# Kernel tuning notes

Hardware: AMD Instinct MI355X
Metric: run time of the kernel (lower is better)

Reference implementation:

```python
import jax, jax.numpy as jnp
import numpy as np

N = 50000   # nodes
E = 600000  # edges (avg degree ~12)
R = 8       # num_relations = 2 * n_speakers**2, n_speakers=2
B = 32      # num_bases = args.batch_size
GD, H1, H2 = 128, 128, 128


def setup_inputs() -> dict:
    key = jax.random.key(0)
    ks = jax.random.split(key, 16)
    w = lambda k, shape: jax.random.normal(k, shape, jnp.float32) * 0.05
    return {
        "node_features": jax.random.normal(ks[0], (N, GD), jnp.float32),
        "edge_index": jax.random.randint(ks[1], (2, E), 0, N),
        "edge_norm": jax.random.uniform(ks[2], (E,), jnp.float32),
        "edge_type": jax.random.randint(ks[3], (E,), 0, R),
        "basis": w(ks[4], (B, GD, H1)),
        "comp": w(ks[5], (R, B)),
        "root": w(ks[6], (GD, H1)),
        "bias1": jnp.zeros((H1,), jnp.float32),
        "w_key": w(ks[7], (H1, H2)),
        "b_key": jnp.zeros((H2,), jnp.float32),
        "w_query": w(ks[8], (H1, H2)),
        "b_query": jnp.zeros((H2,), jnp.float32),
        "w_value": w(ks[9], (H1, H2)),
        "b_value": jnp.zeros((H2,), jnp.float32),
        "w_skip": w(ks[10], (H1, H2)),
        "b_skip": jnp.zeros((H2,), jnp.float32),
    }


def reference(node_features, edge_index, edge_norm, edge_type, basis, comp,
              root, bias1, w_key, b_key, w_query, b_query, w_value, b_value,
              w_skip, b_skip):
    n = node_features.shape[0]
    r = comp.shape[0]
    src, dst = edge_index[0], edge_index[1]

    # ---- RGCNConv (basis decomposition, per-relation mean aggregation) ----
    W = jnp.einsum('rb,bio->rio', comp, basis)            # [R, GD, H1]
    xW = jnp.einsum('ni,rio->rno', node_features, W)      # [R, N, H1]
    msg = xW[edge_type, src]                              # [E, H1]
    seg = edge_type * n + dst                             # combined (relation, dst) segment id
    agg = jax.ops.segment_sum(msg, seg, num_segments=r * n).reshape(r, n, -1)
    cnt = jax.ops.segment_sum(jnp.ones(msg.shape[0], jnp.float32), seg,
                              num_segments=r * n).reshape(r, n, 1)
    h = (agg / jnp.maximum(cnt, 1.0)).sum(0) + node_features @ root + bias1

    # ---- ResGatedGraphConv: sigmoid(k_i + q_j) * v_j, sum-aggregated + skip ----
    k = h @ w_key + b_key
    q = h @ w_query + b_query
    v = h @ w_value + b_value
    m = jax.nn.sigmoid(k[dst] + q[src]) * v[src]          # [E, H2]
    out = jax.ops.segment_sum(m, dst, num_segments=n) + h @ w_skip + b_skip
    return out
```

## Files before the change

### kernel.cpp

```cpp
#include <hip/hip_runtime.h>
#include <stdint.h>

#define GD 128
#define H1 128
#define H2 128
#define NBASES 32
#define NREL 8
#define KZ 1152

typedef __attribute__((ext_vector_type(8))) short bf16x8;
typedef __attribute__((ext_vector_type(4))) float f32x4;

static inline size_t align256(size_t x){ return (x + 255) & ~(size_t)255; }

__device__ __forceinline__ float bf2f(uint32_t u16){
  union { uint32_t u; float f; } c; c.u = (u16 & 0xffffu) << 16; return c.f;
}
__device__ __forceinline__ unsigned short f2bf(float f){
  union { float f; uint32_t u; } c; c.f = f;
  uint32_t u = c.u;
  u += 0x7fffu + ((u >> 16) & 1u);
  return (unsigned short)(u >> 16);
}
__device__ __forceinline__ uint32_t pkbf(float a, float b){
  union { float f; uint32_t u; } ca, cb; ca.f = a; cb.f = b;
  return __builtin_amdgcn_perm(cb.u + 0x8000u, ca.u + 0x8000u, 0x07060302u);
}

__device__ __forceinline__ void async_copy16(void* lds_dst, const void* gsrc){
  __builtin_amdgcn_global_load_lds(
      (const __attribute__((address_space(1))) uint32_t*)gsrc,
      (__attribute__((address_space(3))) uint32_t*)lds_dst, 16, 0, 0);
}

__global__ void k_prep(const float* __restrict__ comp, const float* __restrict__ basis,
                       const float* __restrict__ root, unsigned short* __restrict__ Bz,
                       const float* __restrict__ wk, const float* __restrict__ wq,
                       const float* __restrict__ wv, const float* __restrict__ wsk,
                       const float* __restrict__ bk, const float* __restrict__ bq,
                       const float* __restrict__ bv, const float* __restrict__ bs,
                       unsigned short* __restrict__ B2t, float* __restrict__ Bb,
                       const float4* __restrict__ x, uint2* __restrict__ xout, int cnt4,
                       uint32_t* __restrict__ xpadz, int npadz,
                       const int* __restrict__ edst, const int* __restrict__ etyp,
                       int* __restrict__ cnt, int E, int n){
  int b = blockIdx.x, t = threadIdx.x;
  if (b < 576){
    int idx = b*256 + t;
    int row = idx >> 7, i = idx & 127;
    int r = row >> 7, o = row & 127;
    float v;
    if (r < 8){
      float acc = 0.f;
      #pragma unroll
      for (int bb = 0; bb < NBASES; ++bb)
        acc += comp[r*NBASES + bb] * basis[((size_t)bb*GD + i)*H1 + o];
      v = acc;
    } else {
      v = root[(size_t)i*H1 + o];
    }
    Bz[idx] = f2bf(v);
  } else if (b < 576 + 256){
    int idx = (b - 576)*256 + t;
    int c = idx / H1, k = idx % H1;
    const float* w = (c < 128) ? wk : (c < 256) ? wq : (c < 384) ? wv : wsk;
    B2t[idx] = f2bf(w[(size_t)k*H2 + (c & 127)]);
    if (idx < 512){
      const float* bia = (idx < 128) ? bk : (idx < 256) ? bq : (idx < 384) ? bv : bs;
      Bb[idx] = bia[idx & 127];
    }
  } else {
    int cb = b - (576 + 256);
    int ncastb = (cnt4 + 255) >> 8;
    if (cb < ncastb){
      int i = cb*256 + t;
      if (i < cnt4){
        float4 v = x[i];
        uint2 o; o.x = pkbf(v.x, v.y); o.y = pkbf(v.z, v.w);
        xout[i] = o;
      }
    } else if (cb < ncastb + 12){
      int i = (cb - ncastb)*256 + t;
      if (i < npadz) xpadz[i] = 0u;
    } else {
      int e = (cb - ncastb - 12)*256 + t;
      if (e < E) atomicAdd(&cnt[etyp[e]*n + edst[e]], 1);
    }
  }
}

__global__ void k_scanA(const int* __restrict__ deg, int* __restrict__ off,
                        int* __restrict__ btot, int len){
  __shared__ int wsum[16];
  int t = threadIdx.x, lane = t & 63, w = t >> 6;
  int i0 = blockIdx.x*8192 + t*8;
  int v[8];
  if (i0 + 7 < len){
    int4 va = *(const int4*)(deg + i0);
    int4 vb = *(const int4*)(deg + i0 + 4);
    v[0]=va.x; v[1]=va.y; v[2]=va.z; v[3]=va.w;
    v[4]=vb.x; v[5]=vb.y; v[6]=vb.z; v[7]=vb.w;
  } else {
    #pragma unroll
    for (int u = 0; u < 8; ++u) v[u] = (i0+u < len) ? deg[i0+u] : 0;
  }
  int s[8]; s[0] = v[0];
  #pragma unroll
  for (int u = 1; u < 8; ++u) s[u] = s[u-1] + v[u];
  int x = s[7];
  #pragma unroll
  for (int d = 1; d < 64; d <<= 1){
    int u = __shfl_up(x, d, 64);
    if (lane >= d) x += u;
  }
  if (lane == 63) wsum[w] = x;
  __syncthreads();
  if (t < 16){
    int y = wsum[t];
    #pragma unroll
    for (int d = 1; d < 16; d <<= 1){
      int u = __shfl_up(y, d, 16);
      if (t >= d) y += u;
    }
    wsum[t] = y;
  }
  __syncthreads();
  int woff = (w > 0) ? wsum[w-1] : 0;
  int excl = woff + x - s[7];
  #pragma unroll
  for (int u = 0; u < 8; ++u)
    if (i0+u < len) off[i0+u] = excl + s[u] - v[u];
  if (t == 0) btot[blockIdx.x] = wsum[15];
}

__global__ void k_scanB(const int* __restrict__ btot, int* __restrict__ off,
                        int* __restrict__ cursor, int len, int sentinel){
  int t = threadIdx.x, bid = blockIdx.x;
  int add = 0;
  for (int j = 0; j < bid; ++j) add += btot[j];
  int i0 = bid*8192 + t*8;
  #pragma unroll
  for (int u = 0; u < 8; ++u){
    int i = i0 + u;
    if (i < len){ int val = off[i] + add; off[i] = val; cursor[i] = val; }
  }
  if (bid == 0 && t == 0) off[len] = sentinel;
}

__global__ void k_scatter_rd(const int* __restrict__ src, const int* __restrict__ dst,
                             const int* __restrict__ typ, int* __restrict__ cursor,
                             int* __restrict__ pk, int E, int n){
  int e = blockIdx.x*blockDim.x + threadIdx.x;
  if (e >= E) return;
  int pos = atomicAdd(&cursor[typ[e]*n + dst[e]], 1);
  pk[pos] = src[e];
}

__launch_bounds__(256)
__global__ void k_zgemm(const unsigned short* __restrict__ A, const unsigned short* __restrict__ Bt,
                        unsigned short* __restrict__ Z){
  __shared__ char lds[16384];
  int t = threadIdx.x, lane = t & 63, wave = t >> 6;
  int row0 = blockIdx.x * 128;
  int c0 = blockIdx.y * 128;
  int mrow = lane & 15, quad = lane >> 4;
  int wrow = (wave & 1) * 64, wcol = (wave >> 1) * 64;
  int s = (mrow >> 1) & 3;

  const unsigned short* Asrc = A + (size_t)(row0 + (t >> 2))*H1 + (((t & 3) ^ ((t >> 3) & 3)) << 3);
  const unsigned short* Bsrc = Bt + (size_t)(c0 + (t >> 2))*H1 + (((t & 3) ^ ((t >> 3) & 3)) << 3);
  char* ldsw = lds + wave*1024;

  int aoff = (wrow + mrow)*64 + ((quad ^ s) << 4);
  int boff = 8192 + (wcol + mrow)*64 + ((quad ^ s) << 4);

  f32x4 acc[4][4];
  #pragma unroll
  for (int i = 0; i < 4; ++i)
    #pragma unroll
    for (int j = 0; j < 4; ++j) acc[i][j] = (f32x4){0.f,0.f,0.f,0.f};

  #pragma unroll
  for (int kt = 0; kt < H1; kt += 32){
    __syncthreads();
    async_copy16(ldsw,         Asrc + kt);
    async_copy16(ldsw + 4096,  Asrc + (size_t)64*H1 + kt);
    async_copy16(ldsw + 8192,  Bsrc + kt);
    async_copy16(ldsw + 12288, Bsrc + (size_t)64*H1 + kt);
    __syncthreads();
    bf16x8 af[4], bf[4];
    #pragma unroll
    for (int i = 0; i < 4; ++i) af[i] = *(const bf16x8*)(lds + aoff + i*1024);
    #pragma unroll
    for (int j = 0; j < 4; ++j) bf[j] = *(const bf16x8*)(lds + boff + j*1024);
    #pragma unroll
    for (int i = 0; i < 4; ++i)
      #pragma unroll
      for (int j = 0; j < 4; ++j)
        acc[i][j] = __builtin_amdgcn_mfma_f32_16x16x32_bf16(af[i], bf[j], acc[i][j], 0, 0, 0);
  }
  #pragma unroll
  for (int j = 0; j < 4; ++j){
    int col = c0 + wcol + j*16 + mrow;
    #pragma unroll
    for (int i = 0; i < 4; ++i)
      #pragma unroll
      for (int rg = 0; rg < 4; ++rg){
        int row = row0 + wrow + i*16 + quad*4 + rg;
        Z[(size_t)row*KZ + col] = f2bf(acc[i][j][rg]);
      }
  }
}

__global__ void k_edge1(const int* __restrict__ off_rd, const int* __restrict__ pk_rd,
                        const unsigned short* __restrict__ Zb,
                        const float* __restrict__ bias1,
                        unsigned short* __restrict__ h, int n, int npad){
  int wid = blockIdx.x*(blockDim.x >> 6) + (threadIdx.x >> 6);
  int lane = threadIdx.x & 63;
  if (wid >= npad) return;
  uint32_t* hrow = (uint32_t*)(h + (size_t)wid*H1);
  if (wid >= n){ hrow[lane] = 0u; return; }
  const uint32_t* Z32 = (const uint32_t*)Zb;
  int r8 = lane & 7;
  int o_r = off_rd[(size_t)r8*n + wid];
  int e_r = off_rd[(size_t)r8*n + wid + 1];
  int c_r = e_r - o_r;
  float ic_r = (c_r > 0) ? (1.f/(float)c_r) : 0.f;
  int c0_ = __builtin_amdgcn_readlane(c_r, 0), c1_ = __builtin_amdgcn_readlane(c_r, 1);
  int c2_ = __builtin_amdgcn_readlane(c_r, 2), c3_ = __builtin_amdgcn_readlane(c_r, 3);
  int c4_ = __builtin_amdgcn_readlane(c_r, 4), c5_ = __builtin_amdgcn_readlane(c_r, 5);
  int c6_ = __builtin_amdgcn_readlane(c_r, 6), c7_ = __builtin_amdgcn_readlane(c_r, 7);
  int o0_ = __builtin_amdgcn_readlane(o_r, 0), o1_ = __builtin_amdgcn_readlane(o_r, 1);
  int o2_ = __builtin_amdgcn_readlane(o_r, 2), o3_ = __builtin_amdgcn_readlane(o_r, 3);
  int o4_ = __builtin_amdgcn_readlane(o_r, 4), o5_ = __builtin_amdgcn_readlane(o_r, 5);
  int o6_ = __builtin_amdgcn_readlane(o_r, 6), o7_ = __builtin_amdgcn_readlane(o_r, 7);
  float i0f = __int_as_float(__builtin_amdgcn_readlane(__float_as_int(ic_r), 0));
  float i1f = __int_as_float(__builtin_amdgcn_readlane(__float_as_int(ic_r), 1));
  float i2f = __int_as_float(__builtin_amdgcn_readlane(__float_as_int(ic_r), 2));
  float i3f = __int_as_float(__builtin_amdgcn_readlane(__float_as_int(ic_r), 3));
  float i4f = __int_as_float(__builtin_amdgcn_readlane(__float_as_int(ic_r), 4));
  float i5f = __int_as_float(__builtin_amdgcn_readlane(__float_as_int(ic_r), 5));
  float i6f = __int_as_float(__builtin_amdgcn_readlane(__float_as_int(ic_r), 6));
  float i7f = __int_as_float(__builtin_amdgcn_readlane(__float_as_int(ic_r), 7));
  int p1 = c0_, p2 = p1 + c1_, p3 = p2 + c2_, p4 = p3 + c3_;
  int p5 = p4 + c4_, p6 = p5 + c5_, p7 = p6 + c6_, dg = p7 + c7_;

  float a0 = 0.f, a1 = 0.f;
  for (int jb = 0; jb < dg; jb += 64){
    int i = jb + lane;
    int adj = o0_, rel = 0;
    float wv = i0f;
    adj = (i >= p1) ? (o1_ - p1) : adj;  rel += (i >= p1);  wv = (i >= p1) ? i1f : wv;
    adj = (i >= p2) ? (o2_ - p2) : adj;  rel += (i >= p2);  wv = (i >= p2) ? i2f : wv;
    adj = (i >= p3) ? (o3_ - p3) : adj;  rel += (i >= p3);  wv = (i >= p3) ? i3f : wv;
    adj = (i >= p4) ? (o4_ - p4) : adj;  rel += (i >= p4);  wv = (i >= p4) ? i4f : wv;
    adj = (i >= p5) ? (o5_ - p5) : adj;  rel += (i >= p5);  wv = (i >= p5) ? i5f : wv;
    adj = (i >= p6) ? (o6_ - p6) : adj;  rel += (i >= p6);  wv = (i >= p6) ? i6f : wv;
    adj = (i >= p7) ? (o7_ - p7) : adj;  rel += (i >= p7);  wv = (i >= p7) ? i7f : wv;
    int m = dg - jb; if (m > 64) m = 64;
    int pj = (lane < m) ? pk_rd[adj + i] : 0;
    int gidx = pj*(KZ/2) + rel*64;
    int jj = 0;
    for (; jj + 8 <= m; jj += 8){
      uint32_t g[8]; float wgt[8];
      #pragma unroll
      for (int k = 0; k < 8; ++k){
        int gx = __builtin_amdgcn_readlane(gidx, jj + k);
        wgt[k] = __int_as_float(__builtin_amdgcn_readlane(__float_as_int(wv), jj + k));
        g[k] = Z32[(size_t)(uint32_t)gx + lane];
      }
      #pragma unroll
      for (int k = 0; k < 8; ++k){
        a0 += bf2f(g[k]) * wgt[k];
        a1 += bf2f(g[k] >> 16) * wgt[k];
      }
    }
    for (; jj + 4 <= m; jj += 4){
      uint32_t g[4]; float wgt[4];
      #pragma unroll
      for (int k = 0; k < 4; ++k){
        int gx = __builtin_amdgcn_readlane(gidx, jj + k);
        wgt[k] = __int_as_float(__builtin_amdgcn_readlane(__float_as_int(wv), jj + k));
        g[k] = Z32[(size_t)(uint32_t)gx + lane];
      }
      #pragma unroll
      for (int k = 0; k < 4; ++k){
        a0 += bf2f(g[k]) * wgt[k];
        a1 += bf2f(g[k] >> 16) * wgt[k];
      }
    }
    for (; jj < m; ++jj){
      int gx = __builtin_amdgcn_readlane(gidx, jj);
      float wg = __int_as_float(__builtin_amdgcn_readlane(__float_as_int(wv), jj));
      uint32_t gg = Z32[(size_t)(uint32_t)gx + lane];
      a0 += bf2f(gg) * wg;
      a1 += bf2f(gg >> 16) * wg;
    }
  }
  uint32_t zr = Z32[(size_t)wid*(KZ/2) + 512 + lane];
  float2 bb = ((const float2*)bias1)[lane];
  hrow[lane] = pkbf(a0 + bf2f(zr) + bb.x, a1 + bf2f(zr >> 16) + bb.y);
}

__launch_bounds__(256)
__global__ void k_gemm2(const unsigned short* __restrict__ A, const unsigned short* __restrict__ Bt,
                        const float* __restrict__ Bb, unsigned short* __restrict__ kqv,
                        unsigned short* __restrict__ skipb, int n){
  __shared__ char lds[16384];
  int t = threadIdx.x, lane = t & 63, wave = t >> 6;
  int row0 = blockIdx.x * 128;
  int c0 = blockIdx.y * 128;
  int mrow = lane & 15, quad = lane >> 4;
  int wrow = (wave & 1) * 64, wcol = (wave >> 1) * 64;
  int s = (mrow >> 1) & 3;

  const unsigned short* Asrc = A + (size_t)(row0 + (t >> 2))*H1 + (((t & 3) ^ ((t >> 3) & 3)) << 3);
  const unsigned short* Bsrc = Bt + (size_t)(c0 + (t >> 2))*H1 + (((t & 3) ^ ((t >> 3) & 3)) << 3);
  char* ldsw = lds + wave*1024;

  int aoff = (wrow + mrow)*64 + ((quad ^ s) << 4);
  int boff = 8192 + (wcol + mrow)*64 + ((quad ^ s) << 4);

  f32x4 acc[4][4];
  #pragma unroll
  for (int i = 0; i < 4; ++i)
    #pragma unroll
    for (int j = 0; j < 4; ++j) acc[i][j] = (f32x4){0.f,0.f,0.f,0.f};

  #pragma unroll
  for (int kt = 0; kt < H1; kt += 32){
    __syncthreads();
    async_copy16(ldsw,         Asrc + kt);
    async_copy16(ldsw + 4096,  Asrc + (size_t)64*H1 + kt);
    async_copy16(ldsw + 8192,  Bsrc + kt);
    async_copy16(ldsw + 12288, Bsrc + (size_t)64*H1 + kt);
    __syncthreads();
    bf16x8 af[4], bf[4];
    #pragma unroll
    for (int i = 0; i < 4; ++i) af[i] = *(const bf16x8*)(lds + aoff + i*1024);
    #pragma unroll
    for (int j = 0; j < 4; ++j) bf[j] = *(const bf16x8*)(lds + boff + j*1024);
    #pragma unroll
    for (int i = 0; i < 4; ++i)
      #pragma unroll
      for (int j = 0; j < 4; ++j)
        acc[i][j] = __builtin_amdgcn_mfma_f32_16x16x32_bf16(af[i], bf[j], acc[i][j], 0, 0, 0);
  }
  #pragma unroll
  for (int j = 0; j < 4; ++j){
    int col = c0 + wcol + j*16 + mrow;
    float bcol = Bb[col];
    #pragma unroll
    for (int i = 0; i < 4; ++i)
      #pragma unroll
      for (int rg = 0; rg < 4; ++rg){
        int rr = row0 + wrow + i*16 + quad*4 + rg;
        if (rr >= n) continue;
        float v = acc[i][j][rg] + bcol;
        if (col < 128){
          kqv[(size_t)rr*384 + col] = f2bf(v);
        } else if (col < 256){
          int jj = col - 128;
          kqv[(size_t)rr*384 + 128 + ((jj >> 1) << 2) + (jj & 1)] = f2bf(v);
        } else if (col < 384){
          int jj = col - 256;
          kqv[(size_t)rr*384 + 128 + ((jj >> 1) << 2) + 2 + (jj & 1)] = f2bf(v);
        } else {
          skipb[(size_t)rr*H2 + (col - 384)] = f2bf(v);
        }
      }
  }
}

__global__ void k_edge2(const int* __restrict__ off_rd, const int* __restrict__ pk_rd,
                        const unsigned short* __restrict__ kqv,
                        const unsigned short* __restrict__ skipb,
                        float* __restrict__ out, int n){
  int wid = blockIdx.x*(blockDim.x >> 6) + (threadIdx.x >> 6);
  int lane = threadIdx.x & 63;
  if (wid >= n) return;
  const uint32_t* kv32 = (const uint32_t*)kqv;
  int r = lane & 7;
  int o_r = off_rd[(size_t)r*n + wid];
  int e_r = off_rd[(size_t)r*n + wid + 1];
  int c_r = e_r - o_r;
  int c0_ = __builtin_amdgcn_readlane(c_r, 0), c1_ = __builtin_amdgcn_readlane(c_r, 1);
  int c2_ = __builtin_amdgcn_readlane(c_r, 2), c3_ = __builtin_amdgcn_readlane(c_r, 3);
  int c4_ = __builtin_amdgcn_readlane(c_r, 4), c5_ = __builtin_amdgcn_readlane(c_r, 5);
  int c6_ = __builtin_amdgcn_readlane(c_r, 6), c7_ = __builtin_amdgcn_readlane(c_r, 7);
  int o0_ = __builtin_amdgcn_readlane(o_r, 0), o1_ = __builtin_amdgcn_readlane(o_r, 1);
  int o2_ = __builtin_amdgcn_readlane(o_r, 2), o3_ = __builtin_amdgcn_readlane(o_r, 3);
  int o4_ = __builtin_amdgcn_readlane(o_r, 4), o5_ = __builtin_amdgcn_readlane(o_r, 5);
  int o6_ = __builtin_amdgcn_readlane(o_r, 6), o7_ = __builtin_amdgcn_readlane(o_r, 7);
  int p1 = c0_, p2 = p1 + c1_, p3 = p2 + c2_, p4 = p3 + c3_;
  int p5 = p4 + c4_, p6 = p5 + c5_, p7 = p6 + c6_, dg = p7 + c7_;

  uint32_t ku = kv32[(size_t)wid*192 + lane];
  float k0 = bf2f(ku), k1 = bf2f(ku >> 16);
  float a0 = 0.f, a1 = 0.f;
  for (int jb = 0; jb < dg; jb += 64){
    int i = jb + lane;
    int adj = o0_;
    adj = (i >= p1) ? (o1_ - p1) : adj;
    adj = (i >= p2) ? (o2_ - p2) : adj;
    adj = (i >= p3) ? (o3_ - p3) : adj;
    adj = (i >= p4) ? (o4_ - p4) : adj;
    adj = (i >= p5) ? (o5_ - p5) : adj;
    adj = (i >= p6) ? (o6_ - p6) : adj;
    adj = (i >= p7) ? (o7_ - p7) : adj;
    int m = dg - jb; if (m > 64) m = 64;
    int pj = (lane < m) ? pk_rd[adj + i] : 0;
    int jj = 0;
    for (; jj + 8 <= m; jj += 8){
      uint2 q[8];
      #pragma unroll
      for (int k = 0; k < 8; ++k){
        int s = __builtin_amdgcn_readlane(pj, jj + k);
        q[k] = *(const uint2*)(kv32 + (size_t)s*192 + 64 + lane*2);
      }
      #pragma unroll
      for (int k = 0; k < 8; ++k){
        float qq0 = bf2f(q[k].x), qq1 = bf2f(q[k].x >> 16);
        float vv0 = bf2f(q[k].y), vv1 = bf2f(q[k].y >> 16);
        float g0 = 1.f / (1.f + __expf(-(k0 + qq0)));
        float g1 = 1.f / (1.f + __expf(-(k1 + qq1)));
        a0 += g0*vv0; a1 += g1*vv1;
      }
    }
    for (; jj + 4 <= m; jj += 4){
      uint2 q[4];
      #pragma unroll
      for (int k = 0; k < 4; ++k){
        int s = __builtin_amdgcn_readlane(pj, jj + k);
        q[k] = *(const uint2*)(kv32 + (size_t)s*192 + 64 + lane*2);
      }
      #pragma unroll
      for (int k = 0; k < 4; ++k){
        float qq0 = bf2f(q[k].x), qq1 = bf2f(q[k].x >> 16);
        float vv0 = bf2f(q[k].y), vv1 = bf2f(q[k].y >> 16);
        float g0 = 1.f / (1.f + __expf(-(k0 + qq0)));
        float g1 = 1.f / (1.f + __expf(-(k1 + qq1)));
        a0 += g0*vv0; a1 += g1*vv1;
      }
    }
    for (; jj < m; ++jj){
      int s = __builtin_amdgcn_readlane(pj, jj);
      uint2 qc = *(const uint2*)(kv32 + (size_t)s*192 + 64 + lane*2);
      float qq0 = bf2f(qc.x), qq1 = bf2f(qc.x >> 16);
      float vv0 = bf2f(qc.y), vv1 = bf2f(qc.y >> 16);
      float g0 = 1.f / (1.f + __expf(-(k0 + qq0)));
      float g1 = 1.f / (1.f + __expf(-(k1 + qq1)));
      a0 += g0*vv0; a1 += g1*vv1;
    }
  }
  uint32_t sk = ((const uint32_t*)skipb)[(size_t)wid*64 + lane];
  float2 cur; cur.x = a0 + bf2f(sk); cur.y = a1 + bf2f(sk >> 16);
  ((float2*)(out + (size_t)wid*H2))[lane] = cur;
}

extern "C" void kernel_launch(void* const* d_in, const int* in_sizes, int n_in,
                              void* d_out, int out_size, void* d_ws, size_t ws_size,
                              hipStream_t stream){
  const float* x     = (const float*)d_in[0];
  const int*   eidx  = (const int*)  d_in[1];
  const int*   etype = (const int*)  d_in[3];
  const float* basis = (const float*)d_in[4];
  const float* comp  = (const float*)d_in[5];
  const float* root  = (const float*)d_in[6];
  const float* bias1 = (const float*)d_in[7];
  const float* wk    = (const float*)d_in[8];
  const float* bk    = (const float*)d_in[9];
  const float* wq    = (const float*)d_in[10];
  const float* bq    = (const float*)d_in[11];
  const float* wv    = (const float*)d_in[12];
  const float* bv    = (const float*)d_in[13];
  const float* wsk   = (const float*)d_in[14];
  const float* bs    = (const float*)d_in[15];
  const int n = in_sizes[0] / GD;
  const int E = in_sizes[3];
  const int npad = (n + 127) & ~127;
  const int* esrc = eidx;
  const int* edst = eidx + E;
  float* out = (float*)d_out;

  char* w = (char*)d_ws;
  size_t off = 0;
  unsigned short* xbf  = (unsigned short*)(w + off); off = align256(off + (size_t)npad*GD*2);
  unsigned short* Zbuf = (unsigned short*)(w + off); off = align256(off + (size_t)npad*KZ*2);
  unsigned short* Bz   = (unsigned short*)(w + off); off = align256(off + (size_t)KZ*H1*2);
  unsigned short* B2t  = (unsigned short*)(w + off); off = align256(off + (size_t)512*H1*2);
  float* Bb            = (float*)(w + off);          off = align256(off + 512*4);
  unsigned short* hbuf = (unsigned short*)(w + off); off = align256(off + (size_t)npad*H1*2);
  unsigned short* kqv  = (unsigned short*)(w + off); off = align256(off + (size_t)n*384*2);
  unsigned short* skipb= (unsigned short*)(w + off); off = align256(off + (size_t)npad*H2*2);
  int* cnt_rd          = (int*)(w + off);            off = align256(off + (size_t)(8*n+4)*4);
  int* off_rd          = (int*)(w + off);            off = align256(off + (size_t)(8*n+1)*4);
  int* cur_rd          = (int*)(w + off);            off = align256(off + (size_t)8*n*4);
  int* btot_rd         = (int*)(w + off);            off = align256(off + 64*4);
  int* pk_rd           = (int*)(w + off);            off = align256(off + (size_t)E*4);

  const int nblk_rd = (8*n + 8191) / 8192;
  const int cnt4 = n*GD/4;
  const int ncastb = (cnt4 + 255)/256;
  const int histb  = (E + 255)/256;
  const int npadz  = (npad - n)*GD/2;

  hipMemsetAsync(cnt_rd, 0, (size_t)8*n*4, stream);

  k_prep<<<576 + 256 + ncastb + 12 + histb, 256, 0, stream>>>(
      comp, basis, root, Bz, wk, wq, wv, wsk, bk, bq, bv, bs, B2t, Bb,
      (const float4*)x, (uint2*)xbf, cnt4,
      (uint32_t*)(xbf + (size_t)n*GD), npadz,
      edst, etype, cnt_rd, E, n);
  k_scanA<<<nblk_rd, 1024, 0, stream>>>(cnt_rd, off_rd, btot_rd, 8*n);
  k_scanB<<<nblk_rd, 1024, 0, stream>>>(btot_rd, off_rd, cur_rd, 8*n, E);
  k_scatter_rd<<<(E + 255)/256, 256, 0, stream>>>(esrc, edst, etype, cur_rd, pk_rd, E, n);
  k_zgemm<<<dim3(npad/128, KZ/128), 256, 0, stream>>>(xbf, Bz, Zbuf);
  k_edge1<<<(npad + 3)/4, 256, 0, stream>>>(off_rd, pk_rd, Zbuf, bias1, hbuf, n, npad);
  k_gemm2<<<dim3(npad/128, 4), 256, 0, stream>>>(hbuf, B2t, Bb, kqv, skipb, n);
  k_edge2<<<(n + 3)/4, 256, 0, stream>>>(off_rd, pk_rd, kqv, skipb, out, n);
}
```

Measured before the change: 383.8 us.

## Aggregate raw features per relation before transform, then single K=1152 GEMM

```diff
diff --git a/kernel.cpp b/kernel.cpp
--- a/kernel.cpp
+++ b/kernel.cpp
@@ -6,7 +6,7 @@
 #define H2 128
 #define NBASES 32
 #define NREL 8
-#define KZ 1152
+#define KA 1152
 
 typedef __attribute__((ext_vector_type(8))) short bf16x8;
 typedef __attribute__((ext_vector_type(4))) float f32x4;
@@ -34,16 +34,16 @@
 }
 
 __global__ void k_prep(const float* __restrict__ comp, const float* __restrict__ basis,
-                       const float* __restrict__ root, unsigned short* __restrict__ Bz,
+                       const float* __restrict__ root, unsigned short* __restrict__ Bht,
                        const float* __restrict__ wk, const float* __restrict__ wq,
                        const float* __restrict__ wv, const float* __restrict__ wsk,
                        const float* __restrict__ bk, const float* __restrict__ bq,
                        const float* __restrict__ bv, const float* __restrict__ bs,
                        unsigned short* __restrict__ B2t, float* __restrict__ Bb,
                        const float4* __restrict__ x, uint2* __restrict__ xout, int cnt4,
-                       uint32_t* __restrict__ xpadz, int npadz,
                        const int* __restrict__ edst, const int* __restrict__ etyp,
                        int* __restrict__ cnt, int E, int n){
+  const float LOG2E = 1.4426950408889634f;
   int b = blockIdx.x, t = threadIdx.x;
   if (b < 576){
     int idx = b*256 + t;
@@ -59,15 +59,19 @@
     } else {
       v = root[(size_t)i*H1 + o];
     }
-    Bz[idx] = f2bf(v);
+    Bht[(size_t)o*KA + r*128 + i] = f2bf(v);
   } else if (b < 576 + 256){
     int idx = (b - 576)*256 + t;
     int c = idx / H1, k = idx % H1;
     const float* w = (c < 128) ? wk : (c < 256) ? wq : (c < 384) ? wv : wsk;
-    B2t[idx] = f2bf(w[(size_t)k*H2 + (c & 127)]);
+    float val = w[(size_t)k*H2 + (c & 127)];
+    if (c < 256) val *= LOG2E;
+    B2t[idx] = f2bf(val);
     if (idx < 512){
       const float* bia = (idx < 128) ? bk : (idx < 256) ? bq : (idx < 384) ? bv : bs;
-      Bb[idx] = bia[idx & 127];
+      float bval = bia[idx & 127];
+      if (idx < 256) bval *= LOG2E;
+      Bb[idx] = bval;
     }
   } else {
     int cb = b - (576 + 256);
@@ -79,11 +83,8 @@
         uint2 o; o.x = pkbf(v.x, v.y); o.y = pkbf(v.z, v.w);
         xout[i] = o;
       }
-    } else if (cb < ncastb + 12){
-      int i = (cb - ncastb)*256 + t;
-      if (i < npadz) xpadz[i] = 0u;
     } else {
-      int e = (cb - ncastb - 12)*256 + t;
+      int e = (cb - ncastb)*256 + t;
       if (e < E) atomicAdd(&cnt[etyp[e]*n + edst[e]], 1);
     }
   }
@@ -156,77 +157,22 @@
   pk[pos] = src[e];
 }
 
-__launch_bounds__(256)
-__global__ void k_zgemm(const unsigned short* __restrict__ A, const unsigned short* __restrict__ Bt,
-                        unsigned short* __restrict__ Z){
-  __shared__ char lds[16384];
-  int t = threadIdx.x, lane = t & 63, wave = t >> 6;
-  int row0 = blockIdx.x * 128;
-  int c0 = blockIdx.y * 128;
-  int mrow = lane & 15, quad = lane >> 4;
-  int wrow = (wave & 1) * 64, wcol = (wave >> 1) * 64;
-  int s = (mrow >> 1) & 3;
-
-  const unsigned short* Asrc = A + (size_t)(row0 + (t >> 2))*H1 + (((t & 3) ^ ((t >> 3) & 3)) << 3);
-  const unsigned short* Bsrc = Bt + (size_t)(c0 + (t >> 2))*H1 + (((t & 3) ^ ((t >> 3) & 3)) << 3);
-  char* ldsw = lds + wave*1024;
-
-  int aoff = (wrow + mrow)*64 + ((quad ^ s) << 4);
-  int boff = 8192 + (wcol + mrow)*64 + ((quad ^ s) << 4);
-
-  f32x4 acc[4][4];
-  #pragma unroll
-  for (int i = 0; i < 4; ++i)
-    #pragma unroll
-    for (int j = 0; j < 4; ++j) acc[i][j] = (f32x4){0.f,0.f,0.f,0.f};
-
-  #pragma unroll
-  for (int kt = 0; kt < H1; kt += 32){
-    __syncthreads();
-    async_copy16(ldsw,         Asrc + kt);
-    async_copy16(ldsw + 4096,  Asrc + (size_t)64*H1 + kt);
-    async_copy16(ldsw + 8192,  Bsrc + kt);
-    async_copy16(ldsw + 12288, Bsrc + (size_t)64*H1 + kt);
-    __syncthreads();
-    bf16x8 af[4], bf[4];
-    #pragma unroll
-    for (int i = 0; i < 4; ++i) af[i] = *(const bf16x8*)(lds + aoff + i*1024);
-    #pragma unroll
-    for (int j = 0; j < 4; ++j) bf[j] = *(const bf16x8*)(lds + boff + j*1024);
-    #pragma unroll
-    for (int i = 0; i < 4; ++i)
-      #pragma unroll
-      for (int j = 0; j < 4; ++j)
-        acc[i][j] = __builtin_amdgcn_mfma_f32_16x16x32_bf16(af[i], bf[j], acc[i][j], 0, 0, 0);
-  }
-  #pragma unroll
-  for (int j = 0; j < 4; ++j){
-    int col = c0 + wcol + j*16 + mrow;
-    #pragma unroll
-    for (int i = 0; i < 4; ++i)
-      #pragma unroll
-      for (int rg = 0; rg < 4; ++rg){
-        int row = row0 + wrow + i*16 + quad*4 + rg;
-        Z[(size_t)row*KZ + col] = f2bf(acc[i][j][rg]);
-      }
-  }
-}
-
-__global__ void k_edge1(const int* __restrict__ off_rd, const int* __restrict__ pk_rd,
-                        const unsigned short* __restrict__ Zb,
-                        const float* __restrict__ bias1,
-                        unsigned short* __restrict__ h, int n, int npad){
+__global__ void k_agg(const int* __restrict__ off_rd, const int* __restrict__ pk_rd,
+                      const uint32_t* __restrict__ x32, unsigned short* __restrict__ A2,
+                      int n, int npad){
   int wid = blockIdx.x*(blockDim.x >> 6) + (threadIdx.x >> 6);
   int lane = threadIdx.x & 63;
   if (wid >= npad) return;
-  uint32_t* hrow = (uint32_t*)(h + (size_t)wid*H1);
-  if (wid >= n){ hrow[lane] = 0u; return; }
-  const uint32_t* Z32 = (const uint32_t*)Zb;
+  uint32_t* arow = (uint32_t*)(A2 + (size_t)wid*KA);
+  if (wid >= n){
+    #pragma unroll
+    for (int u = 0; u < 9; ++u) arow[u*64 + lane] = 0u;
+    return;
+  }
   int r8 = lane & 7;
   int o_r = off_rd[(size_t)r8*n + wid];
   int e_r = off_rd[(size_t)r8*n + wid + 1];
   int c_r = e_r - o_r;
-  float ic_r = (c_r > 0) ? (1.f/(float)c_r) : 0.f;
   int c0_ = __builtin_amdgcn_readlane(c_r, 0), c1_ = __builtin_amdgcn_readlane(c_r, 1);
   int c2_ = __builtin_amdgcn_readlane(c_r, 2), c3_ = __builtin_amdgcn_readlane(c_r, 3);
   int c4_ = __builtin_amdgcn_readlane(c_r, 4), c5_ = __builtin_amdgcn_readlane(c_r, 5);
@@ -235,72 +181,99 @@
   int o2_ = __builtin_amdgcn_readlane(o_r, 2), o3_ = __builtin_amdgcn_readlane(o_r, 3);
   int o4_ = __builtin_amdgcn_readlane(o_r, 4), o5_ = __builtin_amdgcn_readlane(o_r, 5);
   int o6_ = __builtin_amdgcn_readlane(o_r, 6), o7_ = __builtin_amdgcn_readlane(o_r, 7);
-  float i0f = __int_as_float(__builtin_amdgcn_readlane(__float_as_int(ic_r), 0));
-  float i1f = __int_as_float(__builtin_amdgcn_readlane(__float_as_int(ic_r), 1));
-  float i2f = __int_as_float(__builtin_amdgcn_readlane(__float_as_int(ic_r), 2));
-  float i3f = __int_as_float(__builtin_amdgcn_readlane(__float_as_int(ic_r), 3));
-  float i4f = __int_as_float(__builtin_amdgcn_readlane(__float_as_int(ic_r), 4));
-  float i5f = __int_as_float(__builtin_amdgcn_readlane(__float_as_int(ic_r), 5));
-  float i6f = __int_as_float(__builtin_amdgcn_readlane(__float_as_int(ic_r), 6));
-  float i7f = __int_as_float(__builtin_amdgcn_readlane(__float_as_int(ic_r), 7));
-  int p1 = c0_, p2 = p1 + c1_, p3 = p2 + c2_, p4 = p3 + c3_;
-  int p5 = p4 + c4_, p6 = p5 + c5_, p7 = p6 + c6_, dg = p7 + c7_;
-
-  float a0 = 0.f, a1 = 0.f;
-  for (int jb = 0; jb < dg; jb += 64){
-    int i = jb + lane;
-    int adj = o0_, rel = 0;
-    float wv = i0f;
-    adj = (i >= p1) ? (o1_ - p1) : adj;  rel += (i >= p1);  wv = (i >= p1) ? i1f : wv;
-    adj = (i >= p2) ? (o2_ - p2) : adj;  rel += (i >= p2);  wv = (i >= p2) ? i2f : wv;
-    adj = (i >= p3) ? (o3_ - p3) : adj;  rel += (i >= p3);  wv = (i >= p3) ? i3f : wv;
-    adj = (i >= p4) ? (o4_ - p4) : adj;  rel += (i >= p4);  wv = (i >= p4) ? i4f : wv;
-    adj = (i >= p5) ? (o5_ - p5) : adj;  rel += (i >= p5);  wv = (i >= p5) ? i5f : wv;
-    adj = (i >= p6) ? (o6_ - p6) : adj;  rel += (i >= p6);  wv = (i >= p6) ? i6f : wv;
-    adj = (i >= p7) ? (o7_ - p7) : adj;  rel += (i >= p7);  wv = (i >= p7) ? i7f : wv;
-    int m = dg - jb; if (m > 64) m = 64;
-    int pj = (lane < m) ? pk_rd[adj + i] : 0;
-    int gidx = pj*(KZ/2) + rel*64;
-    int jj = 0;
-    for (; jj + 8 <= m; jj += 8){
-      uint32_t g[8]; float wgt[8];
-      #pragma unroll
-      for (int k = 0; k < 8; ++k){
-        int gx = __builtin_amdgcn_readlane(gidx, jj + k);
-        wgt[k] = __int_as_float(__builtin_amdgcn_readlane(__float_as_int(wv), jj + k));
-        g[k] = Z32[(size_t)(uint32_t)gx + lane];
-      }
-      #pragma unroll
-      for (int k = 0; k < 8; ++k){
-        a0 += bf2f(g[k]) * wgt[k];
-        a1 += bf2f(g[k] >> 16) * wgt[k];
-      }
-    }
-    for (; jj + 4 <= m; jj += 4){
-      uint32_t g[4]; float wgt[4];
-      #pragma unroll
-      for (int k = 0; k < 4; ++k){
-        int gx = __builtin_amdgcn_readlane(gidx, jj + k);
-        wgt[k] = __int_as_float(__builtin_amdgcn_readlane(__float_as_int(wv), jj + k));
-        g[k] = Z32[(size_t)(uint32_t)gx + lane];
-      }
-      #pragma unroll
-      for (int k = 0; k < 4; ++k){
-        a0 += bf2f(g[k]) * wgt[k];
-        a1 += bf2f(g[k] >> 16) * wgt[k];
-      }
-    }
-    for (; jj < m; ++jj){
-      int gx = __builtin_amdgcn_readlane(gidx, jj);
-      float wg = __int_as_float(__builtin_amdgcn_readlane(__float_as_int(wv), jj));
-      uint32_t gg = Z32[(size_t)(uint32_t)gx + lane];
-      a0 += bf2f(gg) * wg;
-      a1 += bf2f(gg >> 16) * wg;
-    }
-  }
-  uint32_t zr = Z32[(size_t)wid*(KZ/2) + 512 + lane];
-  float2 bb = ((const float2*)bias1)[lane];
-  hrow[lane] = pkbf(a0 + bf2f(zr) + bb.x, a1 + bf2f(zr >> 16) + bb.y);
+
+#define AGGR(rr, oo, cc)                                                        \
+  {                                                                             \
+    float a0 = 0.f, a1 = 0.f;                                                   \
+    for (int jb = 0; jb < (cc); jb += 64){                                      \
+      int m = (cc) - jb; if (m > 64) m = 64;                                    \
+      int pj = (lane < m) ? pk_rd[(oo) + jb + lane] : 0;                        \
+      int jj = 0;                                                               \
+      for (; jj + 4 <= m; jj += 4){                                             \
+        uint32_t g[4];                                                          \
+        _Pragma("unroll")                                                       \
+        for (int k = 0; k < 4; ++k){                                            \
+          int sN = __builtin_amdgcn_readlane(pj, jj + k);                       \
+          g[k] = x32[(size_t)(uint32_t)sN*64 + lane];                           \
+        }                                                                       \
+        _Pragma("unroll")                                                       \
+        for (int k = 0; k < 4; ++k){ a0 += bf2f(g[k]); a1 += bf2f(g[k] >> 16); }\
+      }                                                                         \
+      for (; jj < m; ++jj){                                                     \
+        int sN = __builtin_amdgcn_readlane(pj, jj);                             \
+        uint32_t g = x32[(size_t)(uint32_t)sN*64 + lane];                       \
+        a0 += bf2f(g); a1 += bf2f(g >> 16);                                     \
+      }                                                                         \
+    }                                                                           \
+    float ic = ((cc) > 0) ? __builtin_amdgcn_rcpf((float)(cc)) : 0.f;           \
+    arow[(rr)*64 + lane] = pkbf(a0*ic, a1*ic);                                  \
+  }
+
+  AGGR(0, o0_, c0_)
+  AGGR(1, o1_, c1_)
+  AGGR(2, o2_, c2_)
+  AGGR(3, o3_, c3_)
+  AGGR(4, o4_, c4_)
+  AGGR(5, o5_, c5_)
+  AGGR(6, o6_, c6_)
+  AGGR(7, o7_, c7_)
+#undef AGGR
+  arow[512 + lane] = x32[(size_t)wid*64 + lane];
+}
+
+__launch_bounds__(256)
+__global__ void k_hgemm(const unsigned short* __restrict__ A, const unsigned short* __restrict__ Bt,
+                        const float* __restrict__ bias1, unsigned short* __restrict__ h){
+  __shared__ char lds[16384];
+  int t = threadIdx.x, lane = t & 63, wave = t >> 6;
+  int row0 = blockIdx.x * 128;
+  int mrow = lane & 15, quad = lane >> 4;
+  int wrow = (wave & 1) * 64, wcol = (wave >> 1) * 64;
+  int s = (mrow >> 1) & 3;
+
+  const unsigned short* Asrc = A + (size_t)(row0 + (t >> 2))*KA + (((t & 3) ^ ((t >> 3) & 3)) << 3);
+  const unsigned short* Bsrc = Bt + (size_t)(t >> 2)*KA + (((t & 3) ^ ((t >> 3) & 3)) << 3);
+  char* ldsw = lds + wave*1024;
+
+  int aoff = (wrow + mrow)*64 + ((quad ^ s) << 4);
+  int boff = 8192 + (wcol + mrow)*64 + ((quad ^ s) << 4);
+
+  f32x4 acc[4][4];
+  #pragma unroll
+  for (int i = 0; i < 4; ++i)
+    #pragma unroll
+    for (int j = 0; j < 4; ++j) acc[i][j] = (f32x4){0.f,0.f,0.f,0.f};
+
+  for (int kt = 0; kt < KA; kt += 32){
+    __syncthreads();
+    async_copy16(ldsw,         Asrc + kt);
+    async_copy16(ldsw + 4096,  Asrc + (size_t)64*KA + kt);
+    async_copy16(ldsw + 8192,  Bsrc + kt);
+    async_copy16(ldsw + 12288, Bsrc + (size_t)64*KA + kt);
+    __syncthreads();
+    bf16x8 af[4], bf[4];
+    #pragma unroll
+    for (int i = 0; i < 4; ++i) af[i] = *(const bf16x8*)(lds + aoff + i*1024);
+    #pragma unroll
+    for (int j = 0; j < 4; ++j) bf[j] = *(const bf16x8*)(lds + boff + j*1024);
+    #pragma unroll
+    for (int i = 0; i < 4; ++i)
+      #pragma unroll
+      for (int j = 0; j < 4; ++j)
+        acc[i][j] = __builtin_amdgcn_mfma_f32_16x16x32_bf16(af[i], bf[j], acc[i][j], 0, 0, 0);
+  }
+  #pragma unroll
+  for (int j = 0; j < 4; ++j){
+    int col = wcol + j*16 + mrow;
+    float bc = bias1[col];
+    #pragma unroll
+    for (int i = 0; i < 4; ++i)
+      #pragma unroll
+      for (int rg = 0; rg < 4; ++rg){
+        int row = row0 + wrow + i*16 + quad*4 + rg;
+        h[(size_t)row*H1 + col] = f2bf(acc[i][j][rg] + bc);
+      }
+  }
 }
 
 __launch_bounds__(256)
@@ -423,8 +396,8 @@
       for (int k = 0; k < 8; ++k){
         float qq0 = bf2f(q[k].x), qq1 = bf2f(q[k].x >> 16);
         float vv0 = bf2f(q[k].y), vv1 = bf2f(q[k].y >> 16);
-        float g0 = 1.f / (1.f + __expf(-(k0 + qq0)));
-        float g1 = 1.f / (1.f + __expf(-(k1 + qq1)));
+        float g0 = __builtin_amdgcn_rcpf(1.f + __builtin_amdgcn_exp2f(-(k0 + qq0)));
+        float g1 = __builtin_amdgcn_rcpf(1.f + __builtin_amdgcn_exp2f(-(k1 + qq1)));
         a0 += g0*vv0; a1 += g1*vv1;
       }
     }
@@ -439,8 +412,8 @@
       for (int k = 0; k < 4; ++k){
         float qq0 = bf2f(q[k].x), qq1 = bf2f(q[k].x >> 16);
         float vv0 = bf2f(q[k].y), vv1 = bf2f(q[k].y >> 16);
-        float g0 = 1.f / (1.f + __expf(-(k0 + qq0)));
-        float g1 = 1.f / (1.f + __expf(-(k1 + qq1)));
+        float g0 = __builtin_amdgcn_rcpf(1.f + __builtin_amdgcn_exp2f(-(k0 + qq0)));
+        float g1 = __builtin_amdgcn_rcpf(1.f + __builtin_amdgcn_exp2f(-(k1 + qq1)));
         a0 += g0*vv0; a1 += g1*vv1;
       }
     }
@@ -449,8 +422,8 @@
       uint2 qc = *(const uint2*)(kv32 + (size_t)s*192 + 64 + lane*2);
       float qq0 = bf2f(qc.x), qq1 = bf2f(qc.x >> 16);
       float vv0 = bf2f(qc.y), vv1 = bf2f(qc.y >> 16);
-      float g0 = 1.f / (1.f + __expf(-(k0 + qq0)));
-      float g1 = 1.f / (1.f + __expf(-(k1 + qq1)));
+      float g0 = __builtin_amdgcn_rcpf(1.f + __builtin_amdgcn_exp2f(-(k0 + qq0)));
+      float g1 = __builtin_amdgcn_rcpf(1.f + __builtin_amdgcn_exp2f(-(k1 + qq1)));
       a0 += g0*vv0; a1 += g1*vv1;
     }
   }
@@ -487,8 +460,8 @@
   char* w = (char*)d_ws;
   size_t off = 0;
   unsigned short* xbf  = (unsigned short*)(w + off); off = align256(off + (size_t)npad*GD*2);
-  unsigned short* Zbuf = (unsigned short*)(w + off); off = align256(off + (size_t)npad*KZ*2);
-  unsigned short* Bz   = (unsigned short*)(w + off); off = align256(off + (size_t)KZ*H1*2);
+  unsigned short* A2   = (unsigned short*)(w + off); off = align256(off + (size_t)npad*KA*2);
+  unsigned short* Bht  = (unsigned short*)(w + off); off = align256(off + (size_t)KA*H1*2);
   unsigned short* B2t  = (unsigned short*)(w + off); off = align256(off + (size_t)512*H1*2);
   float* Bb            = (float*)(w + off);          off = align256(off + 512*4);
   unsigned short* hbuf = (unsigned short*)(w + off); off = align256(off + (size_t)npad*H1*2);
@@ -504,20 +477,18 @@
   const int cnt4 = n*GD/4;
   const int ncastb = (cnt4 + 255)/256;
   const int histb  = (E + 255)/256;
-  const int npadz  = (npad - n)*GD/2;
 
   hipMemsetAsync(cnt_rd, 0, (size_t)8*n*4, stream);
 
-  k_prep<<<576 + 256 + ncastb + 12 + histb, 256, 0, stream>>>(
-      comp, basis, root, Bz, wk, wq, wv, wsk, bk, bq, bv, bs, B2t, Bb,
+  k_prep<<<576 + 256 + ncastb + histb, 256, 0, stream>>>(
+      comp, basis, root, Bht, wk, wq, wv, wsk, bk, bq, bv, bs, B2t, Bb,
       (const float4*)x, (uint2*)xbf, cnt4,
-      (uint32_t*)(xbf + (size_t)n*GD), npadz,
       edst, etype, cnt_rd, E, n);
   k_scanA<<<nblk_rd, 1024, 0, stream>>>(cnt_rd, off_rd, btot_rd, 8*n);
   k_scanB<<<nblk_rd, 1024, 0, stream>>>(btot_rd, off_rd, cur_rd, 8*n, E);
   k_scatter_rd<<<(E + 255)/256, 256, 0, stream>>>(esrc, edst, etype, cur_rd, pk_rd, E, n);
-  k_zgemm<<<dim3(npad/128, KZ/128), 256, 0, stream>>>(xbf, Bz, Zbuf);
-  k_edge1<<<(npad + 3)/4, 256, 0, stream>>>(off_rd, pk_rd, Zbuf, bias1, hbuf, n, npad);
+  k_agg<<<(npad + 3)/4, 256, 0, stream>>>(off_rd, pk_rd, (const uint32_t*)xbf, A2, n, npad);
+  k_hgemm<<<npad/128, 256, 0, stream>>>(A2, Bht, bias1, hbuf);
   k_gemm2<<<dim3(npad/128, 4), 256, 0, stream>>>(hbuf, B2t, Bb, kqv, skipb, n);
   k_edge2<<<(n + 3)/4, 256, 0, stream>>>(off_rd, pk_rd, kqv, skipb, out, n);
 }
```

Result: slower. 391.6 us (+2.0%).
